# Optimization experiments

Measured on AMD Instinct MI355X. Metric: run time of the kernel, lower is better.

Reference implementation:

```python
import jax, jax.numpy as jnp
import numpy as np

EPS = 1e-5

def _layernorm_over(x, axes):
    # torch nn.LayerNorm: biased variance, identity affine (fresh module each call)
    mean = jnp.mean(x, axis=axes, keepdims=True)
    var = jnp.var(x, axis=axes, keepdims=True)
    return (x - mean) * jax.lax.rsqrt(var + EPS)

def setup_inputs() -> dict:
    key = jax.random.key(0)
    k1, k2, k3 = jax.random.split(key, 3)
    N, H, D, L = 4, 8, 64, 2048
    C = 64
    return {
        "query": jax.random.normal(k1, (N, H, D, L), dtype=jnp.float32),
        "key": jax.random.normal(k2, (N, H, D, L), dtype=jnp.float32),
        "value": jax.random.normal(k3, (N, H, C, L), dtype=jnp.float32),
    }

def reference(query, key, value):
    N, H, D, L = query.shape
    C = value.shape[2]
    # [N, H, L, M] similarity matrix (fully materialized; required by global LayerNorm)
    sim = jnp.einsum('bhdl,bhdm->bhlm', query, key)
    # LayerNorm over normalized_shape [H, L, M] -> axes (1,2,3)
    sim = _layernorm_over(sim, (1, 2, 3))
    attn = jax.nn.softmax(sim.astype(jnp.float32), axis=-1)
    # [N, H, C, L]
    rv = jnp.einsum('bhlm,bhdm->bhdl', attn, value)
    rv = rv.reshape(N, H * C, L)
    # LayerNorm over normalized_shape [H*C, L] -> axes (1,2)
    rv = _layernorm_over(rv, (1, 2))
    return jax.nn.gelu(rv, approximate=False)
```

## Files before the change

kernel.cpp:

```cpp
#include <hip/hip_runtime.h>
#include <math.h>

#define NB 4
#define NH 8
#define DD 64
#define LL 2048
#define CC 64
#define QB 128
#define KB 64
#define EPS 1e-5

typedef __attribute__((ext_vector_type(4))) float f32x4;
typedef __attribute__((ext_vector_type(8))) short bf16x8;
typedef __attribute__((ext_vector_type(2))) unsigned int u32x2;
typedef __attribute__((ext_vector_type(4))) unsigned int u32x4;

__device__ __forceinline__ unsigned packtrunc(float a, float b) {
  return __builtin_amdgcn_perm(__builtin_bit_cast(unsigned, b),
                               __builtin_bit_cast(unsigned, a), 0x07060302u);
}
__device__ __forceinline__ bf16x8 pack8(f32x4 a, f32x4 b) {
  u32x4 u = {packtrunc(a[0], a[1]), packtrunc(a[2], a[3]),
             packtrunc(b[0], b[1]), packtrunc(b[2], b[3])};
  return __builtin_bit_cast(bf16x8, u);
}

__device__ __forceinline__ void reduce2_atomic(float s, float ss,
                                               double* dS, double* dSS,
                                               float* red, int nw) {
#pragma unroll
  for (int off = 32; off > 0; off >>= 1) {
    s += __shfl_xor(s, off);
    ss += __shfl_xor(ss, off);
  }
  const int t = threadIdx.x;
  if ((t & 63) == 0) { red[t >> 6] = s; red[8 + (t >> 6)] = ss; }
  __syncthreads();
  if (t == 0) {
    float S = 0.f, SS = 0.f;
    for (int w = 0; w < nw; ++w) { S += red[w]; SS += red[8 + w]; }
    atomicAdd(dS, (double)S);
    atomicAdd(dSS, (double)SS);
  }
}

__global__ __launch_bounds__(512, 1) void gram_kernel(
    const float* __restrict__ qg, const float* __restrict__ kg,
    float* __restrict__ sumv, double* __restrict__ ssqd) {
  __shared__ float lsw[8][2][256];

  const int phys = blockIdx.x;
  const int blk = ((phys & 7) << 6) | (phys >> 3);
  const int bh = blk >> 4;
  const int tile = blk & 15;
  const int ti = tile >> 2, tj = tile & 3;
  const int b = bh >> 3;

  const float* qb = qg + (size_t)bh * DD * LL;
  const float* kb = kg + (size_t)bh * DD * LL;

  const int t = threadIdx.x;
  const int lane = t & 63;
  const int w = t >> 6;
  const int g = lane >> 4;
  const int ln = lane & 15;
  const int ri = ti * 16 + ln, rj = tj * 16 + ln;

  f32x4 aq = {0.f, 0.f, 0.f, 0.f}, ak = {0.f, 0.f, 0.f, 0.f};
  float sq = 0.f, sk = 0.f;

#pragma unroll 1
  for (int st = 0; st < 8; ++st) {
    const int l0 = w * 256 + st * 32 + g * 8;
    f32x4 qi0 = *(const f32x4*)&qb[(size_t)ri * LL + l0];
    f32x4 qi1 = *(const f32x4*)&qb[(size_t)ri * LL + l0 + 4];
    f32x4 qj0 = *(const f32x4*)&qb[(size_t)rj * LL + l0];
    f32x4 qj1 = *(const f32x4*)&qb[(size_t)rj * LL + l0 + 4];
    f32x4 ki0 = *(const f32x4*)&kb[(size_t)ri * LL + l0];
    f32x4 ki1 = *(const f32x4*)&kb[(size_t)ri * LL + l0 + 4];
    f32x4 kj0 = *(const f32x4*)&kb[(size_t)rj * LL + l0];
    f32x4 kj1 = *(const f32x4*)&kb[(size_t)rj * LL + l0 + 4];
    aq = __builtin_amdgcn_mfma_f32_16x16x32_bf16(pack8(qi0, qi1), pack8(qj0, qj1), aq, 0, 0, 0);
    ak = __builtin_amdgcn_mfma_f32_16x16x32_bf16(pack8(ki0, ki1), pack8(kj0, kj1), ak, 0, 0, 0);
    if (ti == tj) {
#pragma unroll
      for (int e = 0; e < 4; ++e) { sq += qi0[e] + qi1[e]; sk += ki0[e] + ki1[e]; }
    }
  }

#pragma unroll
  for (int r = 0; r < 4; ++r) {
    lsw[w][0][(g * 4 + r) * 16 + ln] = aq[r];
    lsw[w][1][(g * 4 + r) * 16 + ln] = ak[r];
  }
  if (ti == tj) {
    sq += __shfl_xor(sq, 16); sq += __shfl_xor(sq, 32);
    sk += __shfl_xor(sk, 16); sk += __shfl_xor(sk, 32);
    if (lane < 16) {
      atomicAdd(&sumv[bh * DD + ti * 16 + ln], sq);
      atomicAdd(&sumv[2048 + bh * DD + ti * 16 + ln], sk);
    }
  }
  __syncthreads();

  float prod = 0.f;
  if (t < 256) {
    float gq = 0.f, gk = 0.f;
#pragma unroll
    for (int ww = 0; ww < 8; ++ww) { gq += lsw[ww][0][t]; gk += lsw[ww][1][t]; }
    prod = gq * gk;
  }
#pragma unroll
  for (int off = 1; off < 64; off <<= 1) prod += __shfl_xor(prod, off);
  if (t < 256 && lane == 0) atomicAdd(&ssqd[b], (double)prod);
}

__global__ void fin_kernel(const double* __restrict__ ssqd,
                           const float* __restrict__ sumv,
                           float* __restrict__ scale2) {
  const int t = threadIdx.x, lane = t & 63, b = t >> 6;
  float part = 0.f;
#pragma unroll
  for (int j = 0; j < 8; ++j) {
    const int idx = j * 64 + lane;
    const int bh = b * 8 + (idx >> 6);
    const int d = idx & 63;
    part += sumv[bh * 64 + d] * sumv[2048 + bh * 64 + d];
  }
#pragma unroll
  for (int off = 1; off < 64; off <<= 1) part += __shfl_xor(part, off);
  if (lane == 0) {
    const double cnt = 33554432.0;
    const double mu = (double)part / cnt;
    const double var = ssqd[b] / cnt - mu * mu;
    scale2[b] = (float)(1.4426950408889634 / sqrt(var + EPS));
  }
}

__global__ __launch_bounds__(256, 2) void attn_kernel(
    const float* __restrict__ qg, const float* __restrict__ kg,
    const float* __restrict__ vg, float* __restrict__ rv,
    const float* __restrict__ scale2,
    double* __restrict__ s2, double* __restrict__ s2sq) {
  __shared__ short kt[KB * DD];
  __shared__ short vt[CC * KB];
  __shared__ short qp[QB * DD];
  __shared__ float red[16];

  const int phys = blockIdx.x;
  const int blk = ((phys & 7) << 6) | (phys >> 3);
  const int lblk = blk & 15;
  const int bh = blk >> 4;
  const int b = bh >> 3;
  const int l0 = lblk * QB;

  const float* qbase = qg + (size_t)bh * DD * LL;
  const float* kbase = kg + (size_t)bh * DD * LL;
  const float* vbase = vg + (size_t)bh * CC * LL;

  const int t = threadIdx.x;
  const int lane = t & 63;
  const int wid = t >> 6;
  const int g = lane >> 4;
  const int ln = lane & 15;
  const float sc2 = scale2[b];

  {
    const int l = t & 127;
    const int db = (t >> 7) << 5;
#pragma unroll
    for (int it = 0; it < 8; ++it) {
      const int d0 = db + it * 4;
      float f0 = qbase[(size_t)(d0 + 0) * LL + l0 + l];
      float f1 = qbase[(size_t)(d0 + 1) * LL + l0 + l];
      float f2 = qbase[(size_t)(d0 + 2) * LL + l0 + l];
      float f3 = qbase[(size_t)(d0 + 3) * LL + l0 + l];
      u32x2 wq = {packtrunc(f0, f1), packtrunc(f2, f3)};
      *(u32x2*)&qp[(l * DD + d0) ^ ((l & 7) << 3)] = wq;
    }
  }
  __syncthreads();

  bf16x8 qf[2][2];
#pragma unroll
  for (int rb = 0; rb < 2; ++rb)
#pragma unroll
    for (int kc = 0; kc < 2; ++kc) {
      const int l = wid * 32 + rb * 16 + ln;
      qf[rb][kc] = *(const bf16x8*)&qp[(l * DD + kc * 32 + g * 8) ^ ((l & 7) << 3)];
    }

  short* pw = qp + wid * 2048;

  f32x4 o[2][4];
#pragma unroll
  for (int rb = 0; rb < 2; ++rb)
#pragma unroll
    for (int cf = 0; cf < 4; ++cf) o[rb][cf] = (f32x4){0.f, 0.f, 0.f, 0.f};
  float lacc[2] = {0.f, 0.f};

  float kr[2][16];
  f32x4 vr[2][4];

  auto LOADT = [&](int cur, int mt) {
    const int m0 = mt * KB;
    const int m = t & 63;
    const int db2 = wid * 4;
#pragma unroll
    for (int it = 0; it < 4; ++it) {
      const int d0 = it * 16 + db2;
#pragma unroll
      for (int j = 0; j < 4; ++j)
        kr[cur][it * 4 + j] = kbase[(size_t)(d0 + j) * LL + m0 + m];
    }
    const int cb = t >> 4;
    const int m4 = (t & 15) * 4;
#pragma unroll
    for (int it = 0; it < 4; ++it)
      vr[cur][it] = *(const f32x4*)&vbase[(size_t)(it * 16 + cb) * LL + m0 + m4];
  };

  auto CVTW = [&](int cur) {
    const int m = t & 63;
    const int db2 = wid * 4;
#pragma unroll
    for (int it = 0; it < 4; ++it) {
      const int d0 = it * 16 + db2;
      u32x2 wk = {packtrunc(kr[cur][it * 4 + 0], kr[cur][it * 4 + 1]),
                  packtrunc(kr[cur][it * 4 + 2], kr[cur][it * 4 + 3])};
      *(u32x2*)&kt[(m * DD + d0) ^ ((m & 7) << 3)] = wk;
    }
    const int cb = t >> 4;
    const int m4 = (t & 15) * 4;
#pragma unroll
    for (int it = 0; it < 4; ++it) {
      const int cc = it * 16 + cb;
      f32x4 f = vr[cur][it];
      u32x2 wv = {packtrunc(f[0], f[1]), packtrunc(f[2], f[3])};
      *(u32x2*)&vt[(cc * KB + m4) ^ ((cc & 7) << 3)] = wv;
    }
  };

  auto COMPUTE = [&]() {
    f32x4 s[2][4];
#pragma unroll
    for (int mf = 0; mf < 4; ++mf) {
      const int m = mf * 16 + ln;
      const bf16x8 ka = *(const bf16x8*)&kt[(m * DD + g * 8) ^ ((m & 7) << 3)];
      const bf16x8 kb2 = *(const bf16x8*)&kt[(m * DD + 32 + g * 8) ^ ((m & 7) << 3)];
      f32x4 z = {0.f, 0.f, 0.f, 0.f};
      s[0][mf] = __builtin_amdgcn_mfma_f32_16x16x32_bf16(ka, qf[0][0], z, 0, 0, 0);
      s[0][mf] = __builtin_amdgcn_mfma_f32_16x16x32_bf16(kb2, qf[0][1], s[0][mf], 0, 0, 0);
      s[1][mf] = __builtin_amdgcn_mfma_f32_16x16x32_bf16(ka, qf[1][0], z, 0, 0, 0);
      s[1][mf] = __builtin_amdgcn_mfma_f32_16x16x32_bf16(kb2, qf[1][1], s[1][mf], 0, 0, 0);
    }
#pragma unroll
    for (int rb = 0; rb < 2; ++rb) {
      const int rr = rb * 16 + ln;
#pragma unroll
      for (int mf = 0; mf < 4; ++mf) {
        f32x4 p;
#pragma unroll
        for (int r = 0; r < 4; ++r) {
          p[r] = __builtin_exp2f(s[rb][mf][r] * sc2);
          lacc[rb] += p[r];
        }
        u32x2 wp = {packtrunc(p[0], p[1]), packtrunc(p[2], p[3])};
        *(u32x2*)&pw[(rr * KB + mf * 16 + g * 4) ^ ((rr & 7) << 3)] = wp;
      }
    }
    asm volatile("s_waitcnt lgkmcnt(0)" ::: "memory");
    __builtin_amdgcn_sched_barrier(0);
#pragma unroll
    for (int mk = 0; mk < 2; ++mk) {
      bf16x8 pf[2];
#pragma unroll
      for (int rb = 0; rb < 2; ++rb) {
        const int rr = rb * 16 + ln;
        pf[rb] = *(const bf16x8*)&pw[(rr * KB + mk * 32 + g * 8) ^ ((rr & 7) << 3)];
      }
#pragma unroll
      for (int cf = 0; cf < 4; ++cf) {
        const int c = cf * 16 + ln;
        const bf16x8 vf = *(const bf16x8*)&vt[(c * KB + mk * 32 + g * 8) ^ ((c & 7) << 3)];
        o[0][cf] = __builtin_amdgcn_mfma_f32_16x16x32_bf16(pf[0], vf, o[0][cf], 0, 0, 0);
        o[1][cf] = __builtin_amdgcn_mfma_f32_16x16x32_bf16(pf[1], vf, o[1][cf], 0, 0, 0);
      }
    }
  };

  LOADT(0, 0);
#pragma unroll 1
  for (int mt2 = 0; mt2 < 16; ++mt2) {
    __builtin_amdgcn_s_barrier();
    asm volatile("" ::: "memory");
    CVTW(0);
    LOADT(1, mt2 * 2 + 1);
    __builtin_amdgcn_sched_barrier(0);
    asm volatile("s_waitcnt lgkmcnt(0)" ::: "memory");
    __builtin_amdgcn_s_barrier();
    asm volatile("" ::: "memory");
    COMPUTE();
    __builtin_amdgcn_s_barrier();
    asm volatile("" ::: "memory");
    CVTW(1);
    if (mt2 < 15) LOADT(0, mt2 * 2 + 2);
    __builtin_amdgcn_sched_barrier(0);
    asm volatile("s_waitcnt lgkmcnt(0)" ::: "memory");
    __builtin_amdgcn_s_barrier();
    asm volatile("" ::: "memory");
    COMPUTE();
  }

  float inv[2][4];
#pragma unroll
  for (int rb = 0; rb < 2; ++rb) {
    float ls = lacc[rb];
    ls += __shfl_xor(ls, 16);
    ls += __shfl_xor(ls, 32);
#pragma unroll
    for (int r = 0; r < 4; ++r) inv[rb][r] = 1.0f / __shfl(ls, g * 4 + r);
  }

  float ssum = 0.f, ssq = 0.f;
#pragma unroll
  for (int rb = 0; rb < 2; ++rb) {
    const int lout = l0 + wid * 32 + rb * 16 + g * 4;
#pragma unroll
    for (int cf = 0; cf < 4; ++cf) {
      f32x4 ov;
#pragma unroll
      for (int r = 0; r < 4; ++r) {
        const float x = o[rb][cf][r] * inv[rb][r];
        ov[r] = x;
        ssum += x;
        ssq += x * x;
      }
      *(f32x4*)&rv[((size_t)(bh * CC + cf * 16 + ln)) * LL + lout] = ov;
    }
  }
  __syncthreads();
  reduce2_atomic(ssum, ssq, &s2[b], &s2sq[b], red, 4);
}

__global__ __launch_bounds__(256) void ln_gelu_kernel(
    float* __restrict__ out, const double* __restrict__ s2,
    const double* __restrict__ s2sq) {
  const size_t i = ((size_t)blockIdx.x * 256 + threadIdx.x) * 4;
  const int b = (int)(i >> 20);
  const double cnt = (double)(NH * CC) * (double)LL;
  const double mean = s2[b] / cnt;
  const double var = s2sq[b] / cnt - mean * mean;
  const float invs = (float)(1.0 / sqrt(var + EPS));
  const float mu = (float)mean;
  f32x4 x = *(f32x4*)&out[i];
#pragma unroll
  for (int r = 0; r < 4; ++r) {
    const float z = (x[r] - mu) * invs;
    x[r] = 0.5f * z * (1.0f + erff(z * 0.70710678118f));
  }
  *(f32x4*)&out[i] = x;
}

extern "C" void kernel_launch(void* const* d_in, const int* in_sizes, int n_in,
                              void* d_out, int out_size, void* d_ws, size_t ws_size,
                              hipStream_t stream) {
  (void)in_sizes; (void)n_in; (void)out_size; (void)ws_size;
  const float* q = (const float*)d_in[0];
  const float* k = (const float*)d_in[1];
  const float* v = (const float*)d_in[2];
  float* out = (float*)d_out;

  double* dssq = (double*)d_ws;
  double* ds2 = dssq + 4;
  double* ds2sq = dssq + 8;
  float* sumv = (float*)(dssq + 12);
  float* scale2 = sumv + 4096;

  hipMemsetAsync(d_ws, 0, 12 * 8 + 4096 * 4 + 4 * 4, stream);

  gram_kernel<<<dim3(512), dim3(512), 0, stream>>>(q, k, sumv, dssq);
  fin_kernel<<<dim3(1), dim3(256), 0, stream>>>(dssq, sumv, scale2);
  attn_kernel<<<dim3(512), dim3(256), 0, stream>>>(q, k, v, out, scale2, ds2, ds2sq);
  ln_gelu_kernel<<<dim3((NB * NH * CC * LL) / (4 * 256)), dim3(256), 0, stream>>>(out, ds2, ds2sq);
}
```

Baseline: 203.1 us.

## Restructure gram kernel per head with LDS staging; widen attention blocks to 512 threads

The gram kernel now runs one block per (batch, head) over 32 blocks. It stages bf16 Q and K chunks in LDS and computes the full 64x64 Gram matrices from there, with per-row sums gathered in shared memory, replacing 512 blocks that each reloaded global data. The attention kernel moves to 512 threads with 16 query rows per wave, folds the softmax scale into Q before the bf16 cast, and computes the row sums of P with an MFMA against a ones vector instead of scalar accumulation. The gram change risks low occupancy, since only 32 blocks run across the GPU, and the attention change trades per-wave reuse for more parallelism.

```diff
diff --git a/kernel.cpp b/kernel.cpp
--- a/kernel.cpp
+++ b/kernel.cpp
@@ -19,11 +19,6 @@
   return __builtin_amdgcn_perm(__builtin_bit_cast(unsigned, b),
                                __builtin_bit_cast(unsigned, a), 0x07060302u);
 }
-__device__ __forceinline__ bf16x8 pack8(f32x4 a, f32x4 b) {
-  u32x4 u = {packtrunc(a[0], a[1]), packtrunc(a[2], a[3]),
-             packtrunc(b[0], b[1]), packtrunc(b[2], b[3])};
-  return __builtin_bit_cast(bf16x8, u);
-}
 
 __device__ __forceinline__ void reduce2_atomic(float s, float ss,
                                                double* dS, double* dSS,
@@ -46,16 +41,13 @@
 
 __global__ __launch_bounds__(512, 1) void gram_kernel(
     const float* __restrict__ qg, const float* __restrict__ kg,
-    float* __restrict__ sumv, double* __restrict__ ssqd) {
-  __shared__ float lsw[8][2][256];
-
-  const int phys = blockIdx.x;
-  const int blk = ((phys & 7) << 6) | (phys >> 3);
-  const int bh = blk >> 4;
-  const int tile = blk & 15;
-  const int ti = tile >> 2, tj = tile & 3;
+    double* __restrict__ ssqd, double* __restrict__ musum) {
+  __shared__ short qs[64 * 256];
+  __shared__ short ks[64 * 256];
+  __shared__ float sumbuf[128];
+
+  const int bh = blockIdx.x;
   const int b = bh >> 3;
-
   const float* qb = qg + (size_t)bh * DD * LL;
   const float* kb = kg + (size_t)bh * DD * LL;
 
@@ -64,80 +56,107 @@
   const int w = t >> 6;
   const int g = lane >> 4;
   const int ln = lane & 15;
-  const int ri = ti * 16 + ln, rj = tj * 16 + ln;
-
-  f32x4 aq = {0.f, 0.f, 0.f, 0.f}, ak = {0.f, 0.f, 0.f, 0.f};
-  float sq = 0.f, sk = 0.f;
+
+  if (t < 128) sumbuf[t] = 0.f;
+
+  const int d = t >> 3;
+  const int lseg = (t & 7) * 32;
+  const int ti = w >> 1;
+  const int tj0 = (w & 1) * 2;
+
+  f32x4 aq[2] = {{0.f,0.f,0.f,0.f},{0.f,0.f,0.f,0.f}};
+  f32x4 ak[2] = {{0.f,0.f,0.f,0.f},{0.f,0.f,0.f,0.f}};
 
 #pragma unroll 1
-  for (int st = 0; st < 8; ++st) {
-    const int l0 = w * 256 + st * 32 + g * 8;
-    f32x4 qi0 = *(const f32x4*)&qb[(size_t)ri * LL + l0];
-    f32x4 qi1 = *(const f32x4*)&qb[(size_t)ri * LL + l0 + 4];
-    f32x4 qj0 = *(const f32x4*)&qb[(size_t)rj * LL + l0];
-    f32x4 qj1 = *(const f32x4*)&qb[(size_t)rj * LL + l0 + 4];
-    f32x4 ki0 = *(const f32x4*)&kb[(size_t)ri * LL + l0];
-    f32x4 ki1 = *(const f32x4*)&kb[(size_t)ri * LL + l0 + 4];
-    f32x4 kj0 = *(const f32x4*)&kb[(size_t)rj * LL + l0];
-    f32x4 kj1 = *(const f32x4*)&kb[(size_t)rj * LL + l0 + 4];
-    aq = __builtin_amdgcn_mfma_f32_16x16x32_bf16(pack8(qi0, qi1), pack8(qj0, qj1), aq, 0, 0, 0);
-    ak = __builtin_amdgcn_mfma_f32_16x16x32_bf16(pack8(ki0, ki1), pack8(kj0, kj1), ak, 0, 0, 0);
-    if (ti == tj) {
-#pragma unroll
-      for (int e = 0; e < 4; ++e) { sq += qi0[e] + qi1[e]; sk += ki0[e] + ki1[e]; }
-    }
-  }
-
-#pragma unroll
-  for (int r = 0; r < 4; ++r) {
-    lsw[w][0][(g * 4 + r) * 16 + ln] = aq[r];
-    lsw[w][1][(g * 4 + r) * 16 + ln] = ak[r];
-  }
-  if (ti == tj) {
-    sq += __shfl_xor(sq, 16); sq += __shfl_xor(sq, 32);
-    sk += __shfl_xor(sk, 16); sk += __shfl_xor(sk, 32);
-    if (lane < 16) {
-      atomicAdd(&sumv[bh * DD + ti * 16 + ln], sq);
-      atomicAdd(&sumv[2048 + bh * DD + ti * 16 + ln], sk);
-    }
-  }
+  for (int ch = 0; ch < 8; ++ch) {
+    __syncthreads();
+    float partq = 0.f, partk = 0.f;
+    {
+      const float* src = qb + (size_t)d * LL + ch * 256 + lseg;
+      f32x4 v[8];
+#pragma unroll
+      for (int j = 0; j < 8; ++j) v[j] = *(const f32x4*)&src[j * 4];
+#pragma unroll
+      for (int j = 0; j < 8; ++j)
+#pragma unroll
+        for (int e = 0; e < 4; ++e) partq += v[j][e];
+#pragma unroll
+      for (int j2 = 0; j2 < 4; ++j2) {
+        u32x4 wv = {packtrunc(v[2*j2][0], v[2*j2][1]), packtrunc(v[2*j2][2], v[2*j2][3]),
+                    packtrunc(v[2*j2+1][0], v[2*j2+1][1]), packtrunc(v[2*j2+1][2], v[2*j2+1][3])};
+        *(u32x4*)&qs[(d * 256 + lseg + j2 * 8) ^ ((d & 7) << 3)] = wv;
+      }
+    }
+    {
+      const float* src = kb + (size_t)d * LL + ch * 256 + lseg;
+      f32x4 v[8];
+#pragma unroll
+      for (int j = 0; j < 8; ++j) v[j] = *(const f32x4*)&src[j * 4];
+#pragma unroll
+      for (int j = 0; j < 8; ++j)
+#pragma unroll
+        for (int e = 0; e < 4; ++e) partk += v[j][e];
+#pragma unroll
+      for (int j2 = 0; j2 < 4; ++j2) {
+        u32x4 wv = {packtrunc(v[2*j2][0], v[2*j2][1]), packtrunc(v[2*j2][2], v[2*j2][3]),
+                    packtrunc(v[2*j2+1][0], v[2*j2+1][1]), packtrunc(v[2*j2+1][2], v[2*j2+1][3])};
+        *(u32x4*)&ks[(d * 256 + lseg + j2 * 8) ^ ((d & 7) << 3)] = wv;
+      }
+    }
+    partq += __shfl_xor(partq, 1); partq += __shfl_xor(partq, 2); partq += __shfl_xor(partq, 4);
+    partk += __shfl_xor(partk, 1); partk += __shfl_xor(partk, 2); partk += __shfl_xor(partk, 4);
+    if ((t & 7) == 0) { atomicAdd(&sumbuf[d], partq); atomicAdd(&sumbuf[64 + d], partk); }
+    __syncthreads();
+
+#pragma unroll
+    for (int kc = 0; kc < 8; ++kc) {
+      const int off = kc * 32 + g * 8;
+      const int sw = (ln & 7) << 3;
+      const int ra = ti * 16 + ln;
+      const bf16x8 faq = *(const bf16x8*)&qs[(ra * 256 + off) ^ sw];
+      const bf16x8 fak = *(const bf16x8*)&ks[(ra * 256 + off) ^ sw];
+      const bf16x8 fbq0 = *(const bf16x8*)&qs[((tj0 * 16 + ln) * 256 + off) ^ sw];
+      const bf16x8 fbq1 = *(const bf16x8*)&qs[(((tj0 + 1) * 16 + ln) * 256 + off) ^ sw];
+      const bf16x8 fbk0 = *(const bf16x8*)&ks[((tj0 * 16 + ln) * 256 + off) ^ sw];
+      const bf16x8 fbk1 = *(const bf16x8*)&ks[(((tj0 + 1) * 16 + ln) * 256 + off) ^ sw];
+      aq[0] = __builtin_amdgcn_mfma_f32_16x16x32_bf16(faq, fbq0, aq[0], 0, 0, 0);
+      aq[1] = __builtin_amdgcn_mfma_f32_16x16x32_bf16(faq, fbq1, aq[1], 0, 0, 0);
+      ak[0] = __builtin_amdgcn_mfma_f32_16x16x32_bf16(fak, fbk0, ak[0], 0, 0, 0);
+      ak[1] = __builtin_amdgcn_mfma_f32_16x16x32_bf16(fak, fbk1, ak[1], 0, 0, 0);
+    }
+  }
+
+  float prod = 0.f;
+#pragma unroll
+  for (int ip = 0; ip < 2; ++ip)
+#pragma unroll
+    for (int r = 0; r < 4; ++r) prod += aq[ip][r] * ak[ip][r];
+#pragma unroll
+  for (int off = 1; off < 64; off <<= 1) prod += __shfl_xor(prod, off);
+  if (lane == 0) atomicAdd(&ssqd[b], (double)prod);
+
   __syncthreads();
-
-  float prod = 0.f;
-  if (t < 256) {
-    float gq = 0.f, gk = 0.f;
-#pragma unroll
-    for (int ww = 0; ww < 8; ++ww) { gq += lsw[ww][0][t]; gk += lsw[ww][1][t]; }
-    prod = gq * gk;
-  }
-#pragma unroll
-  for (int off = 1; off < 64; off <<= 1) prod += __shfl_xor(prod, off);
-  if (t < 256 && lane == 0) atomicAdd(&ssqd[b], (double)prod);
+  if (t < 64) {
+    float pr = sumbuf[t] * sumbuf[64 + t];
+#pragma unroll
+    for (int off = 1; off < 64; off <<= 1) pr += __shfl_xor(pr, off);
+    if (t == 0) atomicAdd(&musum[b], (double)pr);
+  }
 }
 
 __global__ void fin_kernel(const double* __restrict__ ssqd,
-                           const float* __restrict__ sumv,
+                           const double* __restrict__ musum,
                            float* __restrict__ scale2) {
-  const int t = threadIdx.x, lane = t & 63, b = t >> 6;
-  float part = 0.f;
-#pragma unroll
-  for (int j = 0; j < 8; ++j) {
-    const int idx = j * 64 + lane;
-    const int bh = b * 8 + (idx >> 6);
-    const int d = idx & 63;
-    part += sumv[bh * 64 + d] * sumv[2048 + bh * 64 + d];
-  }
-#pragma unroll
-  for (int off = 1; off < 64; off <<= 1) part += __shfl_xor(part, off);
-  if (lane == 0) {
+  const int b = threadIdx.x;
+  if (b < NB) {
     const double cnt = 33554432.0;
-    const double mu = (double)part / cnt;
+    const double mu = musum[b] / cnt;
     const double var = ssqd[b] / cnt - mu * mu;
     scale2[b] = (float)(1.4426950408889634 / sqrt(var + EPS));
   }
 }
 
-__global__ __launch_bounds__(256, 2) void attn_kernel(
+__global__ __launch_bounds__(512, 4) void attn_kernel(
     const float* __restrict__ qg, const float* __restrict__ kg,
     const float* __restrict__ vg, float* __restrict__ rv,
     const float* __restrict__ scale2,
@@ -167,74 +186,66 @@
 
   {
     const int l = t & 127;
-    const int db = (t >> 7) << 5;
-#pragma unroll
-    for (int it = 0; it < 8; ++it) {
-      const int d0 = db + it * 4;
-      float f0 = qbase[(size_t)(d0 + 0) * LL + l0 + l];
-      float f1 = qbase[(size_t)(d0 + 1) * LL + l0 + l];
-      float f2 = qbase[(size_t)(d0 + 2) * LL + l0 + l];
-      float f3 = qbase[(size_t)(d0 + 3) * LL + l0 + l];
+    const int db = (t >> 7) << 4;
+#pragma unroll
+    for (int j = 0; j < 4; ++j) {
+      const int d0 = db + j * 4;
+      float f0 = qbase[(size_t)(d0 + 0) * LL + l0 + l] * sc2;
+      float f1 = qbase[(size_t)(d0 + 1) * LL + l0 + l] * sc2;
+      float f2 = qbase[(size_t)(d0 + 2) * LL + l0 + l] * sc2;
+      float f3 = qbase[(size_t)(d0 + 3) * LL + l0 + l] * sc2;
       u32x2 wq = {packtrunc(f0, f1), packtrunc(f2, f3)};
       *(u32x2*)&qp[(l * DD + d0) ^ ((l & 7) << 3)] = wq;
     }
   }
   __syncthreads();
 
-  bf16x8 qf[2][2];
-#pragma unroll
-  for (int rb = 0; rb < 2; ++rb)
-#pragma unroll
-    for (int kc = 0; kc < 2; ++kc) {
-      const int l = wid * 32 + rb * 16 + ln;
-      qf[rb][kc] = *(const bf16x8*)&qp[(l * DD + kc * 32 + g * 8) ^ ((l & 7) << 3)];
-    }
-
-  short* pw = qp + wid * 2048;
-
-  f32x4 o[2][4];
-#pragma unroll
-  for (int rb = 0; rb < 2; ++rb)
-#pragma unroll
-    for (int cf = 0; cf < 4; ++cf) o[rb][cf] = (f32x4){0.f, 0.f, 0.f, 0.f};
-  float lacc[2] = {0.f, 0.f};
-
-  float kr[2][16];
-  f32x4 vr[2][4];
+  bf16x8 qf[2];
+#pragma unroll
+  for (int kc = 0; kc < 2; ++kc) {
+    const int l = wid * 16 + ln;
+    qf[kc] = *(const bf16x8*)&qp[(l * DD + kc * 32 + g * 8) ^ ((ln & 7) << 3)];
+  }
+
+  short* pw = qp + wid * 1024;
+
+  f32x4 o[4];
+#pragma unroll
+  for (int cf = 0; cf < 4; ++cf) o[cf] = (f32x4){0.f, 0.f, 0.f, 0.f};
+  f32x4 dacc = {0.f, 0.f, 0.f, 0.f};
+
+  const unsigned one2 = 0x3F803F80u;
+  const u32x4 onesu = {one2, one2, one2, one2};
+  const bf16x8 ones = __builtin_bit_cast(bf16x8, onesu);
+
+  float kr[2][8];
+  f32x4 vr[2][2];
 
   auto LOADT = [&](int cur, int mt) {
     const int m0 = mt * KB;
     const int m = t & 63;
-    const int db2 = wid * 4;
-#pragma unroll
-    for (int it = 0; it < 4; ++it) {
-      const int d0 = it * 16 + db2;
-#pragma unroll
-      for (int j = 0; j < 4; ++j)
-        kr[cur][it * 4 + j] = kbase[(size_t)(d0 + j) * LL + m0 + m];
-    }
+    const int d0 = (t >> 6) * 8;
+#pragma unroll
+    for (int j = 0; j < 8; ++j)
+      kr[cur][j] = kbase[(size_t)(d0 + j) * LL + m0 + m];
     const int cb = t >> 4;
     const int m4 = (t & 15) * 4;
 #pragma unroll
-    for (int it = 0; it < 4; ++it)
-      vr[cur][it] = *(const f32x4*)&vbase[(size_t)(it * 16 + cb) * LL + m0 + m4];
+    for (int it = 0; it < 2; ++it)
+      vr[cur][it] = *(const f32x4*)&vbase[(size_t)(it * 32 + cb) * LL + m0 + m4];
   };
 
   auto CVTW = [&](int cur) {
     const int m = t & 63;
-    const int db2 = wid * 4;
-#pragma unroll
-    for (int it = 0; it < 4; ++it) {
-      const int d0 = it * 16 + db2;
-      u32x2 wk = {packtrunc(kr[cur][it * 4 + 0], kr[cur][it * 4 + 1]),
-                  packtrunc(kr[cur][it * 4 + 2], kr[cur][it * 4 + 3])};
-      *(u32x2*)&kt[(m * DD + d0) ^ ((m & 7) << 3)] = wk;
-    }
+    const int d0 = (t >> 6) * 8;
+    u32x4 wk = {packtrunc(kr[cur][0], kr[cur][1]), packtrunc(kr[cur][2], kr[cur][3]),
+                packtrunc(kr[cur][4], kr[cur][5]), packtrunc(kr[cur][6], kr[cur][7])};
+    *(u32x4*)&kt[(m * DD + d0) ^ ((m & 7) << 3)] = wk;
     const int cb = t >> 4;
     const int m4 = (t & 15) * 4;
 #pragma unroll
-    for (int it = 0; it < 4; ++it) {
-      const int cc = it * 16 + cb;
+    for (int it = 0; it < 2; ++it) {
+      const int cc = it * 32 + cb;
       f32x4 f = vr[cur][it];
       u32x2 wv = {packtrunc(f[0], f[1]), packtrunc(f[2], f[3])};
       *(u32x2*)&vt[(cc * KB + m4) ^ ((cc & 7) << 3)] = wv;
@@ -242,49 +253,35 @@
   };
 
   auto COMPUTE = [&]() {
-    f32x4 s[2][4];
+    f32x4 s[4];
 #pragma unroll
     for (int mf = 0; mf < 4; ++mf) {
       const int m = mf * 16 + ln;
       const bf16x8 ka = *(const bf16x8*)&kt[(m * DD + g * 8) ^ ((m & 7) << 3)];
       const bf16x8 kb2 = *(const bf16x8*)&kt[(m * DD + 32 + g * 8) ^ ((m & 7) << 3)];
       f32x4 z = {0.f, 0.f, 0.f, 0.f};
-      s[0][mf] = __builtin_amdgcn_mfma_f32_16x16x32_bf16(ka, qf[0][0], z, 0, 0, 0);
-      s[0][mf] = __builtin_amdgcn_mfma_f32_16x16x32_bf16(kb2, qf[0][1], s[0][mf], 0, 0, 0);
-      s[1][mf] = __builtin_amdgcn_mfma_f32_16x16x32_bf16(ka, qf[1][0], z, 0, 0, 0);
-      s[1][mf] = __builtin_amdgcn_mfma_f32_16x16x32_bf16(kb2, qf[1][1], s[1][mf], 0, 0, 0);
-    }
-#pragma unroll
-    for (int rb = 0; rb < 2; ++rb) {
-      const int rr = rb * 16 + ln;
-#pragma unroll
-      for (int mf = 0; mf < 4; ++mf) {
-        f32x4 p;
-#pragma unroll
-        for (int r = 0; r < 4; ++r) {
-          p[r] = __builtin_exp2f(s[rb][mf][r] * sc2);
-          lacc[rb] += p[r];
-        }
-        u32x2 wp = {packtrunc(p[0], p[1]), packtrunc(p[2], p[3])};
-        *(u32x2*)&pw[(rr * KB + mf * 16 + g * 4) ^ ((rr & 7) << 3)] = wp;
-      }
+      s[mf] = __builtin_amdgcn_mfma_f32_16x16x32_bf16(ka, qf[0], z, 0, 0, 0);
+      s[mf] = __builtin_amdgcn_mfma_f32_16x16x32_bf16(kb2, qf[1], s[mf], 0, 0, 0);
+    }
+#pragma unroll
+    for (int mf = 0; mf < 4; ++mf) {
+      f32x4 p;
+#pragma unroll
+      for (int r = 0; r < 4; ++r) p[r] = __builtin_exp2f(s[mf][r]);
+      u32x2 wp = {packtrunc(p[0], p[1]), packtrunc(p[2], p[3])};
+      *(u32x2*)&pw[(ln * KB + mf * 16 + g * 4) ^ ((ln & 7) << 3)] = wp;
     }
     asm volatile("s_waitcnt lgkmcnt(0)" ::: "memory");
     __builtin_amdgcn_sched_barrier(0);
 #pragma unroll
     for (int mk = 0; mk < 2; ++mk) {
-      bf16x8 pf[2];
-#pragma unroll
-      for (int rb = 0; rb < 2; ++rb) {
-        const int rr = rb * 16 + ln;
-        pf[rb] = *(const bf16x8*)&pw[(rr * KB + mk * 32 + g * 8) ^ ((rr & 7) << 3)];
-      }
+      const bf16x8 pf = *(const bf16x8*)&pw[(ln * KB + mk * 32 + g * 8) ^ ((ln & 7) << 3)];
+      dacc = __builtin_amdgcn_mfma_f32_16x16x32_bf16(pf, ones, dacc, 0, 0, 0);
 #pragma unroll
       for (int cf = 0; cf < 4; ++cf) {
         const int c = cf * 16 + ln;
-        const bf16x8 vf = *(const bf16x8*)&vt[(c * KB + mk * 32 + g * 8) ^ ((c & 7) << 3)];
-        o[0][cf] = __builtin_amdgcn_mfma_f32_16x16x32_bf16(pf[0], vf, o[0][cf], 0, 0, 0);
-        o[1][cf] = __builtin_amdgcn_mfma_f32_16x16x32_bf16(pf[1], vf, o[1][cf], 0, 0, 0);
+        const bf16x8 vf = *(const bf16x8*)&vt[(c * KB + mk * 32 + g * 8) ^ ((ln & 7) << 3)];
+        o[cf] = __builtin_amdgcn_mfma_f32_16x16x32_bf16(pf, vf, o[cf], 0, 0, 0);
       }
     }
   };
@@ -312,35 +309,26 @@
     COMPUTE();
   }
 
-  float inv[2][4];
-#pragma unroll
-  for (int rb = 0; rb < 2; ++rb) {
-    float ls = lacc[rb];
-    ls += __shfl_xor(ls, 16);
-    ls += __shfl_xor(ls, 32);
-#pragma unroll
-    for (int r = 0; r < 4; ++r) inv[rb][r] = 1.0f / __shfl(ls, g * 4 + r);
-  }
+  float inv[4];
+#pragma unroll
+  for (int r = 0; r < 4; ++r) inv[r] = 1.0f / dacc[r];
 
   float ssum = 0.f, ssq = 0.f;
-#pragma unroll
-  for (int rb = 0; rb < 2; ++rb) {
-    const int lout = l0 + wid * 32 + rb * 16 + g * 4;
-#pragma unroll
-    for (int cf = 0; cf < 4; ++cf) {
-      f32x4 ov;
-#pragma unroll
-      for (int r = 0; r < 4; ++r) {
-        const float x = o[rb][cf][r] * inv[rb][r];
-        ov[r] = x;
-        ssum += x;
-        ssq += x * x;
-      }
-      *(f32x4*)&rv[((size_t)(bh * CC + cf * 16 + ln)) * LL + lout] = ov;
-    }
+  const int lout = l0 + wid * 16 + g * 4;
+#pragma unroll
+  for (int cf = 0; cf < 4; ++cf) {
+    f32x4 ov;
+#pragma unroll
+    for (int r = 0; r < 4; ++r) {
+      const float x = o[cf][r] * inv[r];
+      ov[r] = x;
+      ssum += x;
+      ssq += x * x;
+    }
+    *(f32x4*)&rv[((size_t)(bh * CC + cf * 16 + ln)) * LL + lout] = ov;
   }
   __syncthreads();
-  reduce2_atomic(ssum, ssq, &s2[b], &s2sq[b], red, 4);
+  reduce2_atomic(ssum, ssq, &s2[b], &s2sq[b], red, 8);
 }
 
 __global__ __launch_bounds__(256) void ln_gelu_kernel(
@@ -371,16 +359,16 @@
   const float* v = (const float*)d_in[2];
   float* out = (float*)d_out;
 
-  double* dssq = (double*)d_ws;
-  double* ds2 = dssq + 4;
-  double* ds2sq = dssq + 8;
-  float* sumv = (float*)(dssq + 12);
-  float* scale2 = sumv + 4096;
-
-  hipMemsetAsync(d_ws, 0, 12 * 8 + 4096 * 4 + 4 * 4, stream);
-
-  gram_kernel<<<dim3(512), dim3(512), 0, stream>>>(q, k, sumv, dssq);
-  fin_kernel<<<dim3(1), dim3(256), 0, stream>>>(dssq, sumv, scale2);
-  attn_kernel<<<dim3(512), dim3(256), 0, stream>>>(q, k, v, out, scale2, ds2, ds2sq);
+  double* ssqd = (double*)d_ws;
+  double* musum = ssqd + 4;
+  double* ds2 = ssqd + 8;
+  double* ds2sq = ssqd + 12;
+  float* scale2 = (float*)(ssqd + 16);
+
+  hipMemsetAsync(d_ws, 0, 16 * 8 + 4 * 4, stream);
+
+  gram_kernel<<<dim3(32), dim3(512), 0, stream>>>(q, k, ssqd, musum);
+  fin_kernel<<<dim3(1), dim3(64), 0, stream>>>(ssqd, musum, scale2);
+  attn_kernel<<<dim3(512), dim3(512), 0, stream>>>(q, k, v, out, scale2, ds2, ds2sq);
   ln_gelu_kernel<<<dim3((NB * NH * CC * LL) / (4 * 256)), dim3(256), 0, stream>>>(out, ds2, ds2sq);
 }
```

New measurement: 204.7 us. Within noise of the previous version (+0.8%).

## Split Gram stats into two kernels and double-buffer attention K/V tiles

Applied to the files above, without the earlier changes.

The Gram statistics pass is split into two kernels. The first computes per-chunk 64x64 Q and K Gram partials through LDS-staged MFMA and writes them into the output buffer as scratch; the second reduces them across chunks. The attention kernel double-buffers the K/V shared tiles so conversion of the next tile overlaps compute and fewer barriers are needed per step. It also folds the softmax scale into Q at load, computes row sums with an MFMA against a ones vector, and raises wave priority around the MFMA sections. The costs are an extra kernel launch, more LDS per block, and row sums taken from bf16-truncated probabilities.

```diff
diff --git a/kernel.cpp b/kernel.cpp
--- a/kernel.cpp
+++ b/kernel.cpp
@@ -19,11 +19,6 @@
   return __builtin_amdgcn_perm(__builtin_bit_cast(unsigned, b),
                                __builtin_bit_cast(unsigned, a), 0x07060302u);
 }
-__device__ __forceinline__ bf16x8 pack8(f32x4 a, f32x4 b) {
-  u32x4 u = {packtrunc(a[0], a[1]), packtrunc(a[2], a[3]),
-             packtrunc(b[0], b[1]), packtrunc(b[2], b[3])};
-  return __builtin_bit_cast(bf16x8, u);
-}
 
 __device__ __forceinline__ void reduce2_atomic(float s, float ss,
                                                double* dS, double* dSS,
@@ -44,17 +39,17 @@
   }
 }
 
-__global__ __launch_bounds__(512, 1) void gram_kernel(
+__global__ __launch_bounds__(256, 4) void gram1_kernel(
     const float* __restrict__ qg, const float* __restrict__ kg,
-    float* __restrict__ sumv, double* __restrict__ ssqd) {
-  __shared__ float lsw[8][2][256];
-
-  const int phys = blockIdx.x;
-  const int blk = ((phys & 7) << 6) | (phys >> 3);
+    float* __restrict__ gout, float* __restrict__ colq,
+    float* __restrict__ colk) {
+  __shared__ short qs[64 * 128];
+  __shared__ short ks[64 * 128];
+
+  const int blk = blockIdx.x;
   const int bh = blk >> 4;
-  const int tile = blk & 15;
-  const int ti = tile >> 2, tj = tile & 3;
-  const int b = bh >> 3;
+  const int ch = blk & 15;
+  const int l0 = ch * 128;
 
   const float* qb = qg + (size_t)bh * DD * LL;
   const float* kb = kg + (size_t)bh * DD * LL;
@@ -64,69 +59,122 @@
   const int w = t >> 6;
   const int g = lane >> 4;
   const int ln = lane & 15;
-  const int ri = ti * 16 + ln, rj = tj * 16 + ln;
-
-  f32x4 aq = {0.f, 0.f, 0.f, 0.f}, ak = {0.f, 0.f, 0.f, 0.f};
-  float sq = 0.f, sk = 0.f;
-
+
+  {
+    const int d = t >> 2;
+    const int lseg = (t & 3) * 32;
+    const int swz = (d & 7) << 3;
+    float pq = 0.f, pk = 0.f;
+    f32x4 v[8];
+#pragma unroll
+    for (int j = 0; j < 8; ++j) v[j] = *(const f32x4*)&qb[(size_t)d * LL + l0 + lseg + j * 4];
+#pragma unroll
+    for (int j = 0; j < 8; ++j)
+#pragma unroll
+      for (int e = 0; e < 4; ++e) pq += v[j][e];
+#pragma unroll
+    for (int j2 = 0; j2 < 4; ++j2) {
+      u32x4 wv = {packtrunc(v[2*j2][0], v[2*j2][1]), packtrunc(v[2*j2][2], v[2*j2][3]),
+                  packtrunc(v[2*j2+1][0], v[2*j2+1][1]), packtrunc(v[2*j2+1][2], v[2*j2+1][3])};
+      *(u32x4*)&qs[(d * 128 + lseg + j2 * 8) ^ swz] = wv;
+    }
+#pragma unroll
+    for (int j = 0; j < 8; ++j) v[j] = *(const f32x4*)&kb[(size_t)d * LL + l0 + lseg + j * 4];
+#pragma unroll
+    for (int j = 0; j < 8; ++j)
+#pragma unroll
+      for (int e = 0; e < 4; ++e) pk += v[j][e];
+#pragma unroll
+    for (int j2 = 0; j2 < 4; ++j2) {
+      u32x4 wv = {packtrunc(v[2*j2][0], v[2*j2][1]), packtrunc(v[2*j2][2], v[2*j2][3]),
+                  packtrunc(v[2*j2+1][0], v[2*j2+1][1]), packtrunc(v[2*j2+1][2], v[2*j2+1][3])};
+      *(u32x4*)&ks[(d * 128 + lseg + j2 * 8) ^ swz] = wv;
+    }
+    pq += __shfl_xor(pq, 1); pq += __shfl_xor(pq, 2);
+    pk += __shfl_xor(pk, 1); pk += __shfl_xor(pk, 2);
+    if ((t & 3) == 0) {
+      atomicAdd(&colq[bh * DD + d], pq);
+      atomicAdd(&colk[bh * DD + d], pk);
+    }
+  }
+  __syncthreads();
+
+  f32x4 aq[4] = {{0,0,0,0},{0,0,0,0},{0,0,0,0},{0,0,0,0}};
+  f32x4 ak[4] = {{0,0,0,0},{0,0,0,0},{0,0,0,0},{0,0,0,0}};
+  const int swzl = (ln & 7) << 3;
+#pragma unroll
+  for (int kc = 0; kc < 4; ++kc) {
+    const int off = kc * 32 + g * 8;
+    const bf16x8 faq = *(const bf16x8*)&qs[((w * 16 + ln) * 128 + off) ^ swzl];
+    const bf16x8 fak = *(const bf16x8*)&ks[((w * 16 + ln) * 128 + off) ^ swzl];
+#pragma unroll
+    for (int tj = 0; tj < 4; ++tj) {
+      const bf16x8 fbq = *(const bf16x8*)&qs[((tj * 16 + ln) * 128 + off) ^ swzl];
+      const bf16x8 fbk = *(const bf16x8*)&ks[((tj * 16 + ln) * 128 + off) ^ swzl];
+      aq[tj] = __builtin_amdgcn_mfma_f32_16x16x32_bf16(faq, fbq, aq[tj], 0, 0, 0);
+      ak[tj] = __builtin_amdgcn_mfma_f32_16x16x32_bf16(fak, fbk, ak[tj], 0, 0, 0);
+    }
+  }
+
+  float* gq = gout + ((size_t)(bh * 16 + ch) * 2) * 4096;
+  float* gk = gq + 4096;
+#pragma unroll
+  for (int tj = 0; tj < 4; ++tj) {
+    const int cell = (w * 4 + tj) * 256 + g * 64 + ln;
+#pragma unroll
+    for (int r = 0; r < 4; ++r) {
+      gq[cell + r * 16] = aq[tj][r];
+      gk[cell + r * 16] = ak[tj][r];
+    }
+  }
+}
+
+__global__ __launch_bounds__(256, 4) void gram2_kernel(
+    const float* __restrict__ gout, double* __restrict__ ssqd) {
+  __shared__ float red[8];
+  const int bh = blockIdx.x;
+  const int t = threadIdx.x;
+  const int lane = t & 63;
+
+  const float* base = gout + (size_t)(bh * 16) * 2 * 4096;
+  f32x4 sq[4] = {{0,0,0,0},{0,0,0,0},{0,0,0,0},{0,0,0,0}};
+  f32x4 sk[4] = {{0,0,0,0},{0,0,0,0},{0,0,0,0},{0,0,0,0}};
 #pragma unroll 1
-  for (int st = 0; st < 8; ++st) {
-    const int l0 = w * 256 + st * 32 + g * 8;
-    f32x4 qi0 = *(const f32x4*)&qb[(size_t)ri * LL + l0];
-    f32x4 qi1 = *(const f32x4*)&qb[(size_t)ri * LL + l0 + 4];
-    f32x4 qj0 = *(const f32x4*)&qb[(size_t)rj * LL + l0];
-    f32x4 qj1 = *(const f32x4*)&qb[(size_t)rj * LL + l0 + 4];
-    f32x4 ki0 = *(const f32x4*)&kb[(size_t)ri * LL + l0];
-    f32x4 ki1 = *(const f32x4*)&kb[(size_t)ri * LL + l0 + 4];
-    f32x4 kj0 = *(const f32x4*)&kb[(size_t)rj * LL + l0];
-    f32x4 kj1 = *(const f32x4*)&kb[(size_t)rj * LL + l0 + 4];
-    aq = __builtin_amdgcn_mfma_f32_16x16x32_bf16(pack8(qi0, qi1), pack8(qj0, qj1), aq, 0, 0, 0);
-    ak = __builtin_amdgcn_mfma_f32_16x16x32_bf16(pack8(ki0, ki1), pack8(kj0, kj1), ak, 0, 0, 0);
-    if (ti == tj) {
-#pragma unroll
-      for (int e = 0; e < 4; ++e) { sq += qi0[e] + qi1[e]; sk += ki0[e] + ki1[e]; }
-    }
-  }
-
-#pragma unroll
-  for (int r = 0; r < 4; ++r) {
-    lsw[w][0][(g * 4 + r) * 16 + ln] = aq[r];
-    lsw[w][1][(g * 4 + r) * 16 + ln] = ak[r];
-  }
-  if (ti == tj) {
-    sq += __shfl_xor(sq, 16); sq += __shfl_xor(sq, 32);
-    sk += __shfl_xor(sk, 16); sk += __shfl_xor(sk, 32);
-    if (lane < 16) {
-      atomicAdd(&sumv[bh * DD + ti * 16 + ln], sq);
-      atomicAdd(&sumv[2048 + bh * DD + ti * 16 + ln], sk);
-    }
-  }
+  for (int ch = 0; ch < 16; ++ch) {
+    const float* pq = base + (size_t)ch * 2 * 4096 + t * 16;
+    const float* pk = pq + 4096;
+#pragma unroll
+    for (int i = 0; i < 4; ++i) {
+      f32x4 a = *(const f32x4*)&pq[i * 4];
+      f32x4 b = *(const f32x4*)&pk[i * 4];
+#pragma unroll
+      for (int e = 0; e < 4; ++e) { sq[i][e] += a[e]; sk[i][e] += b[e]; }
+    }
+  }
+  float prod = 0.f;
+#pragma unroll
+  for (int i = 0; i < 4; ++i)
+#pragma unroll
+    for (int e = 0; e < 4; ++e) prod += sq[i][e] * sk[i][e];
+#pragma unroll
+  for (int off = 1; off < 64; off <<= 1) prod += __shfl_xor(prod, off);
+  if (lane == 0) red[t >> 6] = prod;
   __syncthreads();
-
-  float prod = 0.f;
-  if (t < 256) {
-    float gq = 0.f, gk = 0.f;
-#pragma unroll
-    for (int ww = 0; ww < 8; ++ww) { gq += lsw[ww][0][t]; gk += lsw[ww][1][t]; }
-    prod = gq * gk;
-  }
-#pragma unroll
-  for (int off = 1; off < 64; off <<= 1) prod += __shfl_xor(prod, off);
-  if (t < 256 && lane == 0) atomicAdd(&ssqd[b], (double)prod);
+  if (t == 0) {
+    float S = red[0] + red[1] + red[2] + red[3];
+    atomicAdd(&ssqd[bh >> 3], (double)S);
+  }
 }
 
 __global__ void fin_kernel(const double* __restrict__ ssqd,
-                           const float* __restrict__ sumv,
+                           const float* __restrict__ colq,
+                           const float* __restrict__ colk,
                            float* __restrict__ scale2) {
   const int t = threadIdx.x, lane = t & 63, b = t >> 6;
   float part = 0.f;
 #pragma unroll
-  for (int j = 0; j < 8; ++j) {
-    const int idx = j * 64 + lane;
-    const int bh = b * 8 + (idx >> 6);
-    const int d = idx & 63;
-    part += sumv[bh * 64 + d] * sumv[2048 + bh * 64 + d];
-  }
+  for (int j = 0; j < 8; ++j)
+    part += colq[(b * 8 + j) * DD + lane] * colk[(b * 8 + j) * DD + lane];
 #pragma unroll
   for (int off = 1; off < 64; off <<= 1) part += __shfl_xor(part, off);
   if (lane == 0) {
@@ -142,8 +190,8 @@
     const float* __restrict__ vg, float* __restrict__ rv,
     const float* __restrict__ scale2,
     double* __restrict__ s2, double* __restrict__ s2sq) {
-  __shared__ short kt[KB * DD];
-  __shared__ short vt[CC * KB];
+  __shared__ short kt[2][KB * DD];
+  __shared__ short vt[2][CC * KB];
   __shared__ short qp[QB * DD];
   __shared__ float red[16];
 
@@ -168,15 +216,17 @@
   {
     const int l = t & 127;
     const int db = (t >> 7) << 5;
-#pragma unroll
-    for (int it = 0; it < 8; ++it) {
-      const int d0 = db + it * 4;
-      float f0 = qbase[(size_t)(d0 + 0) * LL + l0 + l];
-      float f1 = qbase[(size_t)(d0 + 1) * LL + l0 + l];
-      float f2 = qbase[(size_t)(d0 + 2) * LL + l0 + l];
-      float f3 = qbase[(size_t)(d0 + 3) * LL + l0 + l];
-      u32x2 wq = {packtrunc(f0, f1), packtrunc(f2, f3)};
-      *(u32x2*)&qp[(l * DD + d0) ^ ((l & 7) << 3)] = wq;
+    const int swz = (l & 7) << 3;
+#pragma unroll
+    for (int j2 = 0; j2 < 4; ++j2) {
+      const int d0 = db + j2 * 8;
+      float f[8];
+#pragma unroll
+      for (int j = 0; j < 8; ++j)
+        f[j] = qbase[(size_t)(d0 + j) * LL + l0 + l] * sc2;
+      u32x4 wq = {packtrunc(f[0], f[1]), packtrunc(f[2], f[3]),
+                  packtrunc(f[4], f[5]), packtrunc(f[6], f[7])};
+      *(u32x4*)&qp[(l * DD + d0) ^ swz] = wq;
     }
   }
   __syncthreads();
@@ -197,7 +247,11 @@
   for (int rb = 0; rb < 2; ++rb)
 #pragma unroll
     for (int cf = 0; cf < 4; ++cf) o[rb][cf] = (f32x4){0.f, 0.f, 0.f, 0.f};
-  float lacc[2] = {0.f, 0.f};
+  f32x4 dacc[2] = {{0.f,0.f,0.f,0.f},{0.f,0.f,0.f,0.f}};
+
+  const unsigned one2 = 0x3F803F80u;
+  const u32x4 onesu = {one2, one2, one2, one2};
+  const bf16x8 ones = __builtin_bit_cast(bf16x8, onesu);
 
   float kr[2][16];
   f32x4 vr[2][4];
@@ -205,72 +259,70 @@
   auto LOADT = [&](int cur, int mt) {
     const int m0 = mt * KB;
     const int m = t & 63;
-    const int db2 = wid * 4;
-#pragma unroll
-    for (int it = 0; it < 4; ++it) {
-      const int d0 = it * 16 + db2;
-#pragma unroll
-      for (int j = 0; j < 4; ++j)
-        kr[cur][it * 4 + j] = kbase[(size_t)(d0 + j) * LL + m0 + m];
-    }
-    const int cb = t >> 4;
+    const int d0 = (t >> 6) * 16;
+#pragma unroll
+    for (int j = 0; j < 16; ++j)
+      kr[cur][j] = kbase[(size_t)(d0 + j) * LL + m0 + m];
+    const int c0 = t >> 4;
     const int m4 = (t & 15) * 4;
 #pragma unroll
     for (int it = 0; it < 4; ++it)
-      vr[cur][it] = *(const f32x4*)&vbase[(size_t)(it * 16 + cb) * LL + m0 + m4];
+      vr[cur][it] = *(const f32x4*)&vbase[(size_t)(it * 16 + c0) * LL + m0 + m4];
   };
 
   auto CVTW = [&](int cur) {
     const int m = t & 63;
-    const int db2 = wid * 4;
+    const int d0 = (t >> 6) * 16;
+    const int swz = (m & 7) << 3;
+    u32x4 w0 = {packtrunc(kr[cur][0], kr[cur][1]), packtrunc(kr[cur][2], kr[cur][3]),
+                packtrunc(kr[cur][4], kr[cur][5]), packtrunc(kr[cur][6], kr[cur][7])};
+    u32x4 w1 = {packtrunc(kr[cur][8], kr[cur][9]), packtrunc(kr[cur][10], kr[cur][11]),
+                packtrunc(kr[cur][12], kr[cur][13]), packtrunc(kr[cur][14], kr[cur][15])};
+    *(u32x4*)&kt[cur][(m * DD + d0) ^ swz] = w0;
+    *(u32x4*)&kt[cur][(m * DD + d0 + 8) ^ swz] = w1;
+    const int c0 = t >> 4;
+    const int m4 = (t & 15) * 4;
 #pragma unroll
     for (int it = 0; it < 4; ++it) {
-      const int d0 = it * 16 + db2;
-      u32x2 wk = {packtrunc(kr[cur][it * 4 + 0], kr[cur][it * 4 + 1]),
-                  packtrunc(kr[cur][it * 4 + 2], kr[cur][it * 4 + 3])};
-      *(u32x2*)&kt[(m * DD + d0) ^ ((m & 7) << 3)] = wk;
-    }
-    const int cb = t >> 4;
-    const int m4 = (t & 15) * 4;
-#pragma unroll
-    for (int it = 0; it < 4; ++it) {
-      const int cc = it * 16 + cb;
+      const int cc = it * 16 + c0;
       f32x4 f = vr[cur][it];
       u32x2 wv = {packtrunc(f[0], f[1]), packtrunc(f[2], f[3])};
-      *(u32x2*)&vt[(cc * KB + m4) ^ ((cc & 7) << 3)] = wv;
+      *(u32x2*)&vt[cur][(cc * KB + m4) ^ ((cc & 7) << 3)] = wv;
     }
   };
 
-  auto COMPUTE = [&]() {
+  auto COMPUTE = [&](int cur) {
     f32x4 s[2][4];
+    __builtin_amdgcn_s_setprio(1);
 #pragma unroll
     for (int mf = 0; mf < 4; ++mf) {
       const int m = mf * 16 + ln;
-      const bf16x8 ka = *(const bf16x8*)&kt[(m * DD + g * 8) ^ ((m & 7) << 3)];
-      const bf16x8 kb2 = *(const bf16x8*)&kt[(m * DD + 32 + g * 8) ^ ((m & 7) << 3)];
+      const int swz = (m & 7) << 3;
+      const bf16x8 ka = *(const bf16x8*)&kt[cur][(m * DD + g * 8) ^ swz];
+      const bf16x8 kb2 = *(const bf16x8*)&kt[cur][(m * DD + 32 + g * 8) ^ swz];
       f32x4 z = {0.f, 0.f, 0.f, 0.f};
       s[0][mf] = __builtin_amdgcn_mfma_f32_16x16x32_bf16(ka, qf[0][0], z, 0, 0, 0);
       s[0][mf] = __builtin_amdgcn_mfma_f32_16x16x32_bf16(kb2, qf[0][1], s[0][mf], 0, 0, 0);
       s[1][mf] = __builtin_amdgcn_mfma_f32_16x16x32_bf16(ka, qf[1][0], z, 0, 0, 0);
       s[1][mf] = __builtin_amdgcn_mfma_f32_16x16x32_bf16(kb2, qf[1][1], s[1][mf], 0, 0, 0);
     }
+    __builtin_amdgcn_s_setprio(0);
 #pragma unroll
     for (int rb = 0; rb < 2; ++rb) {
       const int rr = rb * 16 + ln;
+      const int swz = (rr & 7) << 3;
 #pragma unroll
       for (int mf = 0; mf < 4; ++mf) {
         f32x4 p;
 #pragma unroll
-        for (int r = 0; r < 4; ++r) {
-          p[r] = __builtin_exp2f(s[rb][mf][r] * sc2);
-          lacc[rb] += p[r];
-        }
+        for (int r = 0; r < 4; ++r) p[r] = __builtin_exp2f(s[rb][mf][r]);
         u32x2 wp = {packtrunc(p[0], p[1]), packtrunc(p[2], p[3])};
-        *(u32x2*)&pw[(rr * KB + mf * 16 + g * 4) ^ ((rr & 7) << 3)] = wp;
+        *(u32x2*)&pw[(rr * KB + mf * 16 + g * 4) ^ swz] = wp;
       }
     }
     asm volatile("s_waitcnt lgkmcnt(0)" ::: "memory");
     __builtin_amdgcn_sched_barrier(0);
+    __builtin_amdgcn_s_setprio(1);
 #pragma unroll
     for (int mk = 0; mk < 2; ++mk) {
       bf16x8 pf[2];
@@ -279,59 +331,60 @@
         const int rr = rb * 16 + ln;
         pf[rb] = *(const bf16x8*)&pw[(rr * KB + mk * 32 + g * 8) ^ ((rr & 7) << 3)];
       }
+      dacc[0] = __builtin_amdgcn_mfma_f32_16x16x32_bf16(pf[0], ones, dacc[0], 0, 0, 0);
+      dacc[1] = __builtin_amdgcn_mfma_f32_16x16x32_bf16(pf[1], ones, dacc[1], 0, 0, 0);
 #pragma unroll
       for (int cf = 0; cf < 4; ++cf) {
         const int c = cf * 16 + ln;
-        const bf16x8 vf = *(const bf16x8*)&vt[(c * KB + mk * 32 + g * 8) ^ ((c & 7) << 3)];
+        const bf16x8 vf = *(const bf16x8*)&vt[cur][(c * KB + mk * 32 + g * 8) ^ ((c & 7) << 3)];
         o[0][cf] = __builtin_amdgcn_mfma_f32_16x16x32_bf16(pf[0], vf, o[0][cf], 0, 0, 0);
         o[1][cf] = __builtin_amdgcn_mfma_f32_16x16x32_bf16(pf[1], vf, o[1][cf], 0, 0, 0);
       }
     }
+    __builtin_amdgcn_s_setprio(0);
   };
 
   LOADT(0, 0);
+  CVTW(0);
+  LOADT(1, 1);
+  asm volatile("s_waitcnt lgkmcnt(0)" ::: "memory");
+  __builtin_amdgcn_s_barrier();
+  asm volatile("" ::: "memory");
+
 #pragma unroll 1
   for (int mt2 = 0; mt2 < 16; ++mt2) {
-    __builtin_amdgcn_s_barrier();
-    asm volatile("" ::: "memory");
-    CVTW(0);
-    LOADT(1, mt2 * 2 + 1);
+    const int mt = mt2 * 2;
+    CVTW(1);
+    if (mt2 < 15) LOADT(0, mt + 2);
     __builtin_amdgcn_sched_barrier(0);
+    COMPUTE(0);
     asm volatile("s_waitcnt lgkmcnt(0)" ::: "memory");
     __builtin_amdgcn_s_barrier();
     asm volatile("" ::: "memory");
-    COMPUTE();
-    __builtin_amdgcn_s_barrier();
-    asm volatile("" ::: "memory");
-    CVTW(1);
-    if (mt2 < 15) LOADT(0, mt2 * 2 + 2);
-    __builtin_amdgcn_sched_barrier(0);
+    if (mt2 < 15) {
+      CVTW(0);
+      LOADT(1, mt + 3);
+      __builtin_amdgcn_sched_barrier(0);
+    }
+    COMPUTE(1);
     asm volatile("s_waitcnt lgkmcnt(0)" ::: "memory");
     __builtin_amdgcn_s_barrier();
     asm volatile("" ::: "memory");
-    COMPUTE();
-  }
-
-  float inv[2][4];
+  }
+
+  float ssum = 0.f, ssq = 0.f;
 #pragma unroll
   for (int rb = 0; rb < 2; ++rb) {
-    float ls = lacc[rb];
-    ls += __shfl_xor(ls, 16);
-    ls += __shfl_xor(ls, 32);
-#pragma unroll
-    for (int r = 0; r < 4; ++r) inv[rb][r] = 1.0f / __shfl(ls, g * 4 + r);
-  }
-
-  float ssum = 0.f, ssq = 0.f;
-#pragma unroll
-  for (int rb = 0; rb < 2; ++rb) {
+    float inv[4];
+#pragma unroll
+    for (int r = 0; r < 4; ++r) inv[r] = 1.0f / dacc[rb][r];
     const int lout = l0 + wid * 32 + rb * 16 + g * 4;
 #pragma unroll
     for (int cf = 0; cf < 4; ++cf) {
       f32x4 ov;
 #pragma unroll
       for (int r = 0; r < 4; ++r) {
-        const float x = o[rb][cf][r] * inv[rb][r];
+        const float x = o[rb][cf][r] * inv[r];
         ov[r] = x;
         ssum += x;
         ssq += x * x;
@@ -371,16 +424,18 @@
   const float* v = (const float*)d_in[2];
   float* out = (float*)d_out;
 
-  double* dssq = (double*)d_ws;
-  double* ds2 = dssq + 4;
-  double* ds2sq = dssq + 8;
-  float* sumv = (float*)(dssq + 12);
-  float* scale2 = sumv + 4096;
+  double* ssqd = (double*)d_ws;
+  double* ds2 = ssqd + 4;
+  double* ds2sq = ssqd + 8;
+  float* colq = (float*)(ssqd + 12);
+  float* colk = colq + 2048;
+  float* scale2 = colk + 2048;
 
   hipMemsetAsync(d_ws, 0, 12 * 8 + 4096 * 4 + 4 * 4, stream);
 
-  gram_kernel<<<dim3(512), dim3(512), 0, stream>>>(q, k, sumv, dssq);
-  fin_kernel<<<dim3(1), dim3(256), 0, stream>>>(dssq, sumv, scale2);
+  gram1_kernel<<<dim3(512), dim3(256), 0, stream>>>(q, k, out, colq, colk);
+  gram2_kernel<<<dim3(32), dim3(256), 0, stream>>>(out, ssqd);
+  fin_kernel<<<dim3(1), dim3(256), 0, stream>>>(ssqd, colq, colk, scale2);
   attn_kernel<<<dim3(512), dim3(256), 0, stream>>>(q, k, v, out, scale2, ds2, ds2sq);
   ln_gelu_kernel<<<dim3((NB * NH * CC * LL) / (4 * 256)), dim3(256), 0, stream>>>(out, ds2, ds2sq);
 }
```

Result: faster. 179.7 us (-11.5%).
